# Kernel tuning notes

Hardware: AMD Instinct MI355X
Metric: run time of the kernel (lower is better)

## Reference

```python
import jax, jax.numpy as jnp
import numpy as np

B, C, Hs, Ws = 8, 512, 32, 32
NUM_HEADS, D_K = 8, 64
SCALE = D_K ** -0.5


def setup_inputs() -> dict:
    key = jax.random.key(0)
    ks = jax.random.split(key, 8)
    inner = NUM_HEADS * D_K  # 512
    s = 0.02
    return {
        "x": jax.random.normal(ks[0], (B, C, Hs, Ws), dtype=jnp.float32),
        "y": jax.random.normal(ks[1], (B, C, Hs, Ws), dtype=jnp.float32),
        "Wq": jax.random.normal(ks[2], (inner, C), dtype=jnp.float32) * s,
        "bq": jnp.zeros((inner,), dtype=jnp.float32),
        "Wkv": jax.random.normal(ks[3], (2 * inner, C), dtype=jnp.float32) * s,
        "bkv": jnp.zeros((2 * inner,), dtype=jnp.float32),
        "Wp": jax.random.normal(ks[4], (C, inner), dtype=jnp.float32) * s,
        "bp": jnp.zeros((C,), dtype=jnp.float32),
    }


def reference(x, y, Wq, bq, Wkv, bkv, Wp, bp):
    # Faithful to CrossAttentionBlock.forward: y is only shape-checked, unused.
    x_shape = x.shape
    b, c = x.shape[0], x.shape[1]
    # channel_transfer: [B, C, H, W] -> [B, H, W, C] -> [B, N, C]
    xt = jnp.transpose(x, (0, 2, 3, 1)).reshape(b, -1, c)
    n = xt.shape[1]
    # q: [B, N, H*dk] -> [B, H, N, dk]
    q = (xt @ Wq.T + bq).reshape(b, n, NUM_HEADS, D_K).transpose(0, 2, 1, 3)
    # kv: [B, N, 2*H*dk] -> [2, B, H, N, dk]
    kv = (xt @ Wkv.T + bkv).reshape(b, n, 2, NUM_HEADS, D_K).transpose(2, 0, 3, 1, 4)
    k, v = kv[0], kv[1]
    atten = jnp.einsum("bhik,bhjk->bhij", q, k) * SCALE
    atten = jax.nn.softmax(atten, axis=-1)
    res = jnp.einsum("bhij,bhjd->bhid", atten, v)  # [B, H, N, dk]
    res = res.transpose(0, 2, 1, 3).reshape(b, n, NUM_HEADS * D_K)
    res = res @ Wp.T + bp  # [B, N, C]
    # original does a raw reshape of [B, N, C] back into x_shape [B, C, H, W]
    return res.reshape(x_shape)
```

## Files before the change

kernel.cpp:

```cpp
#include <hip/hip_runtime.h>
#include <math.h>

#define BB 8
#define CC 512
#define NH 8
#define DK 64
#define NN 1024
#define MROWS (BB * NN)
#define INNER 512
#define SCALE 0.125f


typedef __attribute__((ext_vector_type(8))) short bf16x8;
typedef __attribute__((ext_vector_type(4))) float floatx4;

__device__ inline short f2bf(float f) {
    union { float f; unsigned u; } un;
    un.f = f;
    unsigned r = un.u + 0x7fffu + ((un.u >> 16) & 1u);
    return (short)(r >> 16);
}

__device__ inline short f2bf_rhu(float f) {
    union { float f; unsigned u; } un;
    un.f = f;
    return (short)((un.u + 0x8000u) >> 16);
}

#define GLD_LDS(gptr, lptr)                                                  \
    __builtin_amdgcn_global_load_lds(                                        \
        (const __attribute__((address_space(1))) void*)(gptr),               \
        (__attribute__((address_space(3))) void*)(lptr), 16, 0, 0)

__global__ __launch_bounds__(256) void prep_kernel(
    const float* __restrict__ x, const float* __restrict__ Wq,
    const float* __restrict__ Wkv, const float* __restrict__ Wp,
    const float* __restrict__ bq, const float* __restrict__ bkv,
    short* __restrict__ xtb, short* __restrict__ wqkvb,
    short* __restrict__ wpb, float* __restrict__ bqkv) {
    __shared__ float tile[32][33];
    const int bid = blockIdx.x;
    if (bid < 4096) {
        const int n0 = (bid & 31) * 32;
        const int c0 = ((bid >> 5) & 15) * 32;
        const int b = bid >> 9;
        const int tx = threadIdx.x & 31;
        const int ty = threadIdx.x >> 5;
        const float* xb = x + (size_t)b * CC * NN;
        short* xo = xtb + (size_t)b * NN * CC;
        for (int i = ty; i < 32; i += 8)
            tile[i][tx] = xb[(size_t)(c0 + i) * NN + n0 + tx];
        __syncthreads();
        for (int i = ty; i < 32; i += 8)
            xo[(size_t)(n0 + i) * CC + c0 + tx] = f2bf(tile[tx][i]);
    } else {
        const int i = (bid - 4096) * 1024 + threadIdx.x * 4;
        if (i < 786432) {
            float4 v = (i < 262144) ? *(const float4*)&Wq[i]
                                    : *(const float4*)&Wkv[i - 262144];
            wqkvb[i + 0] = f2bf(v.x);
            wqkvb[i + 1] = f2bf(v.y);
            wqkvb[i + 2] = f2bf(v.z);
            wqkvb[i + 3] = f2bf(v.w);
        } else if (i < 1048576) {
            const int j = i - 786432;
            float4 v = *(const float4*)&Wp[j];
            wpb[j + 0] = f2bf(v.x);
            wpb[j + 1] = f2bf(v.y);
            wpb[j + 2] = f2bf(v.z);
            wpb[j + 3] = f2bf(v.w);
        } else {
            const int j = i - 1048576;
            if (j < 1536) {
                float4 v = (j < 512) ? *(const float4*)&bq[j]
                                     : *(const float4*)&bkv[j - 512];
                *(float4*)&bqkv[j] = v;
            }
        }
    }
}

template <int MODE, int BN>
__global__ __launch_bounds__(256) void gemm_mfma_kernel(
    const short* __restrict__ A, const short* __restrict__ W,
    const float* __restrict__ bias, float* __restrict__ outf,
    short* __restrict__ outq, short* __restrict__ outk,
    short* __restrict__ outv) {
    constexpr int K = 512;
    constexpr int WCOLS = BN / 64;
    constexpr int WROWS = 4 / WCOLS;
    constexpr int WRSPAN = 128 / WROWS;
    constexpr int RT = WRSPAN / 16;
    constexpr int ABUF = 128 * 32;
    constexpr int BBUF = BN * 32;
    constexpr int STAGE_EL = 2 * ABUF + 2 * BBUF;
    constexpr int CS_EL = (MODE == 1) ? 128 * 132 : 0;
    constexpr int SMEM_EL = (CS_EL > STAGE_EL) ? CS_EL : STAGE_EL;
    __shared__ short smem[SMEM_EL];
    short* As = smem;
    short* Bs = smem + 2 * ABUF;

    const int t = threadIdx.x;
    const int wave = t >> 6;
    const int lane = t & 63;
    const int col = lane & 15;
    const int quad = lane >> 4;
    const int wr = wave / WCOLS;
    const int wc = wave % WCOLS;

    const int bm0 = blockIdx.x * 128;
    const int bn0 = blockIdx.y * BN;

    floatx4 acc[RT][4];
#pragma unroll
    for (int i = 0; i < RT; i++)
#pragma unroll
        for (int j = 0; j < 4; j++) acc[i][j] = (floatx4){0.f, 0.f, 0.f, 0.f};

    const int kpE = (lane & 3) * 8;
    const int rA = wave * 32 + (lane >> 2);
    const short* Ag = A + (size_t)(bm0 + rA) * K + kpE;
    const int rB = wave * (BN / 4) + (lane >> 2);
    const short* Wg = W + (size_t)(bn0 + rB) * K + kpE;
    const int aOff = wave * 1024;
    const int bOff = wave * (BN / 4) * 32;

#define GSTAGE(K0, BUF)                                                       \
    do {                                                                      \
        GLD_LDS(Ag + (K0), As + (BUF)*ABUF + aOff);                           \
        GLD_LDS(Ag + 16 * K + (K0), As + (BUF)*ABUF + aOff + 512);            \
        if constexpr (BN == 128) {                                            \
            GLD_LDS(Wg + (K0), Bs + (BUF)*BBUF + bOff);                       \
            GLD_LDS(Wg + 16 * K + (K0), Bs + (BUF)*BBUF + bOff + 512);        \
        } else {                                                              \
            GLD_LDS(Wg + (K0), Bs + (BUF)*BBUF + bOff);                       \
        }                                                                     \
    } while (0)

    GSTAGE(0, 0);

#pragma unroll
    for (int it = 0; it < 16; it++) {
        const int buf = it & 1;
        __syncthreads();
        if (it < 15) GSTAGE((it + 1) * 32, buf ^ 1);

        const short* A_ = As + buf * ABUF;
        const short* B_ = Bs + buf * BBUF;
        bf16x8 aF[RT], bF[4];
#pragma unroll
        for (int rt = 0; rt < RT; rt++)
            aF[rt] =
                *(const bf16x8*)&A_[(wr * WRSPAN + rt * 16 + col) * 32 + quad * 8];
#pragma unroll
        for (int ct = 0; ct < 4; ct++)
            bF[ct] = *(const bf16x8*)&B_[(wc * 64 + ct * 16 + col) * 32 + quad * 8];
#pragma unroll
        for (int rt = 0; rt < RT; rt++)
#pragma unroll
            for (int ct = 0; ct < 4; ct++)
                acc[rt][ct] = __builtin_amdgcn_mfma_f32_16x16x32_bf16(
                    aF[rt], bF[ct], acc[rt][ct], 0, 0, 0);
    }
#undef GSTAGE

    if (MODE == 1) {
        short* Cs = smem;
        const bool isV = (bn0 >= 1024);
        const bool isQ = (bn0 < 512);
        __syncthreads();
        if (isV) {
#pragma unroll
            for (int rt = 0; rt < RT; rt++) {
#pragma unroll
                for (int ct = 0; ct < 4; ct++) {
                    const int jn_l = wc * 64 + ct * 16 + col;
                    const float bsv = bias[bn0 + jn_l];
                    const int m_l = wr * WRSPAN + rt * 16 + quad * 4;
                    short4 v4;
                    v4.x = f2bf(acc[rt][ct][0] + bsv);
                    v4.y = f2bf(acc[rt][ct][1] + bsv);
                    v4.z = f2bf(acc[rt][ct][2] + bsv);
                    v4.w = f2bf(acc[rt][ct][3] + bsv);
                    *(short4*)&Cs[jn_l * 132 + m_l] = v4;
                }
            }
        } else {
#pragma unroll
            for (int rt = 0; rt < RT; rt++) {
#pragma unroll
                for (int ct = 0; ct < 4; ct++) {
                    const int jn_l = wc * 64 + ct * 16 + col;
                    const float bsv = bias[bn0 + jn_l];
#pragma unroll
                    for (int r = 0; r < 4; r++) {
                        const int m_l = wr * WRSPAN + rt * 16 + quad * 4 + r;
                        const float val = acc[rt][ct][r] + bsv;
                        Cs[m_l * 132 + jn_l] =
                            isQ ? f2bf(val * SCALE) : f2bf(val);
                    }
                }
            }
        }
        __syncthreads();
        const int b = bm0 >> 10;
        const int nbase = bm0 & 1023;
        if (isV) {
#pragma unroll
            for (int p = 0; p < 8; p++) {
                const int cid = p * 256 + t;
                const int jn_l = cid >> 4;
                const int m0 = (cid & 15) * 8;
                bf16x8 frag = *(const bf16x8*)&Cs[jn_l * 132 + m0];
                const int jn_g = bn0 + jn_l;
                const int h = (jn_g >> 6) & 7;
                const int d = jn_g & 63;
                *(bf16x8*)&outv[(((size_t)(b * NH + h)) * DK + d) * NN + nbase +
                                m0] = frag;
            }
        } else {
            short* dst = isQ ? outq : outk;
#pragma unroll
            for (int p = 0; p < 8; p++) {
                const int cid = p * 256 + t;
                const int m_l = cid >> 4;
                const int jn0 = (cid & 15) * 8;
                bf16x8 frag = *(const bf16x8*)&Cs[m_l * 132 + jn0];
                const int jn_g = bn0 + jn0;
                const int h = (jn_g >> 6) & 7;
                const int d = jn_g & 63;
                *(bf16x8*)&dst[(((size_t)(b * NH + h)) * NN + nbase + m_l) * DK +
                               d] = frag;
            }
        }
        return;
    }

#pragma unroll
    for (int rt = 0; rt < RT; rt++) {
#pragma unroll
        for (int ct = 0; ct < 4; ct++) {
            const int jn = bn0 + wc * 64 + ct * 16 + col;
            const float bsv = bias[jn];
#pragma unroll
            for (int r = 0; r < 4; r++) {
                const int m = bm0 + wr * WRSPAN + rt * 16 + quad * 4 + r;
                outf[(size_t)m * 512 + jn] = acc[rt][ct][r] + bsv;
            }
        }
    }
}

__global__ __launch_bounds__(256) void attn_mfma_kernel(
    const short* __restrict__ q, const short* __restrict__ k,
    const short* __restrict__ vt, short* __restrict__ out) {
    const int bh = blockIdx.x;
    const int b = bh >> 3;
    const int h = bh & 7;
    const int n0 = blockIdx.y * 128;
    const int tid = threadIdx.x;
    const int wave = tid >> 6;
    const int lane = tid & 63;
    const int col = lane & 15;
    const int quad = lane >> 4;

    __shared__ short Ks[2][64 * 64];
    __shared__ short Vs[2][64 * 64];
    __shared__ short Ps[4][32][72];

    bf16x8 qa[2][2];
#pragma unroll
    for (int rt = 0; rt < 2; rt++) {
        const size_t qoff =
            ((size_t)bh * NN + n0 + wave * 32 + rt * 16 + col) * DK;
        qa[rt][0] = *(const bf16x8*)&q[qoff + quad * 8];
        qa[rt][1] = *(const bf16x8*)&q[qoff + 32 + quad * 8];
    }

    floatx4 o[2][4];
#pragma unroll
    for (int rt = 0; rt < 2; rt++)
#pragma unroll
        for (int i = 0; i < 4; i++) o[rt][i] = (floatx4){0.f, 0.f, 0.f, 0.f};
    float l_run[2][4] = {{0.f, 0.f, 0.f, 0.f}, {0.f, 0.f, 0.f, 0.f}};

    const short* kg = k + (size_t)bh * NN * DK;
    const short* vg = vt + (size_t)bh * DK * NN;

    const int srow = lane >> 3;
    const int sunit = (lane & 7) ^ srow;
    const int sbase = wave * 16;

    const int xs = col & 7;
    const int pK0 = (quad ^ xs) * 8;
    const int pK1 = ((quad + 4) ^ xs) * 8;

#define STAGE(J0, BUF)                                                         \
    do {                                                                       \
        GLD_LDS(kg + (size_t)((J0) + sbase + srow) * DK + sunit * 8,           \
                &Ks[BUF][sbase * 64]);                                         \
        GLD_LDS(kg + (size_t)((J0) + sbase + 8 + srow) * DK + sunit * 8,       \
                &Ks[BUF][(sbase + 8) * 64]);                                   \
        GLD_LDS(vg + (size_t)(sbase + srow) * NN + (J0) + sunit * 8,           \
                &Vs[BUF][sbase * 64]);                                         \
        GLD_LDS(vg + (size_t)(sbase + 8 + srow) * NN + (J0) + sunit * 8,       \
                &Vs[BUF][(sbase + 8) * 64]);                                   \
    } while (0)

    STAGE(0, 0);

    for (int c = 0; c < 16; c++) {
        const int buf = c & 1;
        __syncthreads();
        if (c < 15) STAGE((c + 1) * 64, buf ^ 1);

        const short* K_ = &Ks[buf][0];
        const short* V_ = &Vs[buf][0];

        float p[2][4][4];
#pragma unroll
        for (int ct = 0; ct < 4; ct++) {
            bf16x8 kb0 = *(const bf16x8*)&K_[(ct * 16 + col) * 64 + pK0];
            bf16x8 kb1 = *(const bf16x8*)&K_[(ct * 16 + col) * 64 + pK1];
#pragma unroll
            for (int rt = 0; rt < 2; rt++) {
                floatx4 acc = (floatx4){0.f, 0.f, 0.f, 0.f};
                acc = __builtin_amdgcn_mfma_f32_16x16x32_bf16(qa[rt][0], kb0,
                                                              acc, 0, 0, 0);
                acc = __builtin_amdgcn_mfma_f32_16x16x32_bf16(qa[rt][1], kb1,
                                                              acc, 0, 0, 0);
#pragma unroll
                for (int r = 0; r < 4; r++) p[rt][ct][r] = __expf(acc[r]);
            }
        }

#pragma unroll
        for (int rt = 0; rt < 2; rt++)
#pragma unroll
            for (int r = 0; r < 4; r++)
                l_run[rt][r] +=
                    (p[rt][0][r] + p[rt][1][r]) + (p[rt][2][r] + p[rt][3][r]);

#pragma unroll
        for (int rt = 0; rt < 2; rt++)
#pragma unroll
            for (int ct = 0; ct < 4; ct++)
#pragma unroll
                for (int r = 0; r < 4; r++)
                    Ps[wave][rt * 16 + quad * 4 + r][ct * 16 + col] =
                        f2bf_rhu(p[rt][ct][r]);

        bf16x8 pa[2][2];
#pragma unroll
        for (int rt = 0; rt < 2; rt++) {
            pa[rt][0] = *(const bf16x8*)&Ps[wave][rt * 16 + col][quad * 8];
            pa[rt][1] = *(const bf16x8*)&Ps[wave][rt * 16 + col][32 + quad * 8];
        }

#pragma unroll
        for (int dt = 0; dt < 4; dt++) {
            bf16x8 vb0 = *(const bf16x8*)&V_[(dt * 16 + col) * 64 + pK0];
            bf16x8 vb1 = *(const bf16x8*)&V_[(dt * 16 + col) * 64 + pK1];
#pragma unroll
            for (int rt = 0; rt < 2; rt++) {
                o[rt][dt] = __builtin_amdgcn_mfma_f32_16x16x32_bf16(
                    pa[rt][0], vb0, o[rt][dt], 0, 0, 0);
                o[rt][dt] = __builtin_amdgcn_mfma_f32_16x16x32_bf16(
                    pa[rt][1], vb1, o[rt][dt], 0, 0, 0);
            }
        }
    }
#undef STAGE

    float inv[2][4];
#pragma unroll
    for (int rt = 0; rt < 2; rt++)
#pragma unroll
        for (int r = 0; r < 4; r++) {
            float lv = l_run[rt][r];
#pragma unroll
            for (int d = 1; d < 16; d <<= 1) lv += __shfl_xor(lv, d, 64);
            inv[rt][r] = 1.f / lv;
        }
#pragma unroll
    for (int rt = 0; rt < 2; rt++)
#pragma unroll
        for (int dt = 0; dt < 4; dt++)
#pragma unroll
            for (int r = 0; r < 4; r++)
                Ps[wave][rt * 16 + quad * 4 + r][dt * 16 + col] =
                    f2bf(o[rt][dt][r] * inv[rt][r]);

#pragma unroll
    for (int rt = 0; rt < 2; rt++) {
        const int row = lane >> 2;
        const int d0 = (lane & 3) * 16;
        bf16x8 f0 = *(const bf16x8*)&Ps[wave][rt * 16 + row][d0];
        bf16x8 f1 = *(const bf16x8*)&Ps[wave][rt * 16 + row][d0 + 8];
        const int m = n0 + wave * 32 + rt * 16 + row;
        short* orow = out + ((size_t)(b * NN + m)) * 512 + h * 64 + d0;
        *(bf16x8*)&orow[0] = f0;
        *(bf16x8*)&orow[8] = f1;
    }
}

extern "C" void kernel_launch(void* const* d_in, const int* in_sizes, int n_in,
                              void* d_out, int out_size, void* d_ws,
                              size_t ws_size, hipStream_t stream) {
    const float* x = (const float*)d_in[0];
    const float* Wq = (const float*)d_in[2];
    const float* bq = (const float*)d_in[3];
    const float* Wkv = (const float*)d_in[4];
    const float* bkv = (const float*)d_in[5];
    const float* Wp = (const float*)d_in[6];
    const float* bp = (const float*)d_in[7];
    float* out = (float*)d_out;

    short* ws = (short*)d_ws;
    short* xtb = ws;
    short* qb = xtb + (size_t)MROWS * CC;
    short* kb = qb + (size_t)MROWS * INNER;
    short* vb = kb + (size_t)MROWS * INNER;
    short* wqkvb = vb + (size_t)MROWS * INNER;
    short* wpb = wqkvb + (size_t)3 * INNER * CC;
    float* bqkv = (float*)(wpb + (size_t)CC * INNER);
    short* att = xtb;

    prep_kernel<<<4096 + 1026, 256, 0, stream>>>(x, Wq, Wkv, Wp, bq, bkv, xtb,
                                                 wqkvb, wpb, bqkv);
    {
        dim3 grid(MROWS / 128, (3 * INNER) / 128);
        gemm_mfma_kernel<1, 128><<<grid, 256, 0, stream>>>(
            xtb, wqkvb, bqkv, nullptr, qb, kb, vb);
    }
    {
        dim3 grid(BB * NH, NN / 128);
        attn_mfma_kernel<<<grid, 256, 0, stream>>>(qb, kb, vb, att);
    }
    {
        dim3 grid(MROWS / 128, CC / 64);
        gemm_mfma_kernel<0, 64><<<grid, 256, 0, stream>>>(
            att, wpb, bp, out, nullptr, nullptr, nullptr);
    }
}
```

Before: 152.1 us.

## Rewrite attention inner loop with 32x32x16 MFMA and register-resident P

The attention kernel switches from 16x16x32 to 32x32x16 bf16 MFMAs and computes S transposed (K times Q), so each lane holds one query column. P is packed to bf16 with v_cvt_pk_bf16_f32 and rearranged across the wave halves with v_permlane32_swap, which removes the LDS round trip through the Ps buffer and its write/read traffic. The softmax scale now folds in log2(e) so exp2 can be used in place of __expf. It relies on gfx950-specific instructions and inline asm, and the final output stores become scalar 2-byte writes instead of 16-byte vector stores.

```diff
diff --git a/kernel.cpp b/kernel.cpp
--- a/kernel.cpp
+++ b/kernel.cpp
@@ -8,11 +8,12 @@
 #define NN 1024
 #define MROWS (BB * NN)
 #define INNER 512
-#define SCALE 0.125f
+#define QSCALE 0.18033688011112042f
 
 
 typedef __attribute__((ext_vector_type(8))) short bf16x8;
 typedef __attribute__((ext_vector_type(4))) float floatx4;
+typedef __attribute__((ext_vector_type(16))) float floatx16;
 
 __device__ inline short f2bf(float f) {
     union { float f; unsigned u; } un;
@@ -21,11 +22,15 @@
     return (short)(r >> 16);
 }
 
-__device__ inline short f2bf_rhu(float f) {
-    union { float f; unsigned u; } un;
-    un.f = f;
-    return (short)((un.u + 0x8000u) >> 16);
-}
+#if defined(__has_builtin)
+#if __has_builtin(__builtin_amdgcn_exp2f)
+#define EXP2(x) __builtin_amdgcn_exp2f(x)
+#else
+#define EXP2(x) __expf((x) * 0.69314718056f)
+#endif
+#else
+#define EXP2(x) __expf((x) * 0.69314718056f)
+#endif
 
 #define GLD_LDS(gptr, lptr)                                                  \
     __builtin_amdgcn_global_load_lds(                                        \
@@ -197,7 +202,7 @@
                         const int m_l = wr * WRSPAN + rt * 16 + quad * 4 + r;
                         const float val = acc[rt][ct][r] + bsv;
                         Cs[m_l * 132 + jn_l] =
-                            isQ ? f2bf(val * SCALE) : f2bf(val);
+                            isQ ? f2bf(val * QSCALE) : f2bf(val);
                     }
                 }
             }
@@ -261,28 +266,28 @@
     const int tid = threadIdx.x;
     const int wave = tid >> 6;
     const int lane = tid & 63;
-    const int col = lane & 15;
-    const int quad = lane >> 4;
+    const int l31 = lane & 31;
+    const int hi = lane >> 5;
+    const int rsw = l31 & 7;
 
     __shared__ short Ks[2][64 * 64];
     __shared__ short Vs[2][64 * 64];
-    __shared__ short Ps[4][32][72];
-
-    bf16x8 qa[2][2];
-#pragma unroll
-    for (int rt = 0; rt < 2; rt++) {
-        const size_t qoff =
-            ((size_t)bh * NN + n0 + wave * 32 + rt * 16 + col) * DK;
-        qa[rt][0] = *(const bf16x8*)&q[qoff + quad * 8];
-        qa[rt][1] = *(const bf16x8*)&q[qoff + 32 + quad * 8];
-    }
-
-    floatx4 o[2][4];
-#pragma unroll
-    for (int rt = 0; rt < 2; rt++)
-#pragma unroll
-        for (int i = 0; i < 4; i++) o[rt][i] = (floatx4){0.f, 0.f, 0.f, 0.f};
-    float l_run[2][4] = {{0.f, 0.f, 0.f, 0.f}, {0.f, 0.f, 0.f, 0.f}};
+
+    bf16x8 qf[4];
+    {
+        const size_t qbase =
+            ((size_t)bh * NN + n0 + wave * 32 + l31) * DK + hi * 8;
+#pragma unroll
+        for (int dc = 0; dc < 4; dc++)
+            qf[dc] = *(const bf16x8*)&q[qbase + dc * 16];
+    }
+
+    floatx16 o[2];
+#pragma unroll
+    for (int dt = 0; dt < 2; dt++)
+#pragma unroll
+        for (int i = 0; i < 16; i++) o[dt][i] = 0.f;
+    float l_run = 0.f;
 
     const short* kg = k + (size_t)bh * NN * DK;
     const short* vg = vt + (size_t)bh * DK * NN;
@@ -290,10 +295,6 @@
     const int srow = lane >> 3;
     const int sunit = (lane & 7) ^ srow;
     const int sbase = wave * 16;
-
-    const int xs = col & 7;
-    const int pK0 = (quad ^ xs) * 8;
-    const int pK1 = ((quad + 4) ^ xs) * 8;
 
 #define STAGE(J0, BUF)                                                         \
     do {                                                                       \
@@ -317,91 +318,89 @@
         const short* K_ = &Ks[buf][0];
         const short* V_ = &Vs[buf][0];
 
-        float p[2][4][4];
-#pragma unroll
-        for (int ct = 0; ct < 4; ct++) {
-            bf16x8 kb0 = *(const bf16x8*)&K_[(ct * 16 + col) * 64 + pK0];
-            bf16x8 kb1 = *(const bf16x8*)&K_[(ct * 16 + col) * 64 + pK1];
-#pragma unroll
-            for (int rt = 0; rt < 2; rt++) {
-                floatx4 acc = (floatx4){0.f, 0.f, 0.f, 0.f};
-                acc = __builtin_amdgcn_mfma_f32_16x16x32_bf16(qa[rt][0], kb0,
-                                                              acc, 0, 0, 0);
-                acc = __builtin_amdgcn_mfma_f32_16x16x32_bf16(qa[rt][1], kb1,
-                                                              acc, 0, 0, 0);
-#pragma unroll
-                for (int r = 0; r < 4; r++) p[rt][ct][r] = __expf(acc[r]);
-            }
-        }
-
-#pragma unroll
-        for (int rt = 0; rt < 2; rt++)
-#pragma unroll
-            for (int r = 0; r < 4; r++)
-                l_run[rt][r] +=
-                    (p[rt][0][r] + p[rt][1][r]) + (p[rt][2][r] + p[rt][3][r]);
-
-#pragma unroll
-        for (int rt = 0; rt < 2; rt++)
-#pragma unroll
-            for (int ct = 0; ct < 4; ct++)
-#pragma unroll
-                for (int r = 0; r < 4; r++)
-                    Ps[wave][rt * 16 + quad * 4 + r][ct * 16 + col] =
-                        f2bf_rhu(p[rt][ct][r]);
-
-        bf16x8 pa[2][2];
-#pragma unroll
-        for (int rt = 0; rt < 2; rt++) {
-            pa[rt][0] = *(const bf16x8*)&Ps[wave][rt * 16 + col][quad * 8];
-            pa[rt][1] = *(const bf16x8*)&Ps[wave][rt * 16 + col][32 + quad * 8];
-        }
-
-#pragma unroll
-        for (int dt = 0; dt < 4; dt++) {
-            bf16x8 vb0 = *(const bf16x8*)&V_[(dt * 16 + col) * 64 + pK0];
-            bf16x8 vb1 = *(const bf16x8*)&V_[(dt * 16 + col) * 64 + pK1];
-#pragma unroll
-            for (int rt = 0; rt < 2; rt++) {
-                o[rt][dt] = __builtin_amdgcn_mfma_f32_16x16x32_bf16(
-                    pa[rt][0], vb0, o[rt][dt], 0, 0, 0);
-                o[rt][dt] = __builtin_amdgcn_mfma_f32_16x16x32_bf16(
-                    pa[rt][1], vb1, o[rt][dt], 0, 0, 0);
-            }
-        }
+        floatx16 sacc[2];
+#pragma unroll
+        for (int kt = 0; kt < 2; kt++) {
+#pragma unroll
+            for (int i = 0; i < 16; i++) sacc[kt][i] = 0.f;
+#pragma unroll
+            for (int dc = 0; dc < 4; dc++) {
+                bf16x8 kf = *(const bf16x8*)&K_[(kt * 32 + l31) * 64 +
+                                                (((dc * 2 + hi) ^ rsw) * 8)];
+                sacc[kt] = __builtin_amdgcn_mfma_f32_32x32x16_bf16(
+                    kf, qf[dc], sacc[kt], 0, 0, 0);
+            }
+        }
+
+        unsigned pw[2][4][2];
+#pragma unroll
+        for (int kt = 0; kt < 2; kt++) {
+            float p[16];
+#pragma unroll
+            for (int i = 0; i < 16; i++) p[i] = EXP2(sacc[kt][i]);
+            float s0 = (p[0] + p[1]) + (p[2] + p[3]);
+            float s1 = (p[4] + p[5]) + (p[6] + p[7]);
+            float s2 = (p[8] + p[9]) + (p[10] + p[11]);
+            float s3 = (p[12] + p[13]) + (p[14] + p[15]);
+            l_run += (s0 + s1) + (s2 + s3);
+#pragma unroll
+            for (int s = 0; s < 4; s++)
+#pragma unroll
+                for (int j = 0; j < 2; j++)
+                    asm("v_cvt_pk_bf16_f32 %0, %1, %2"
+                        : "=v"(pw[kt][s][j])
+                        : "v"(p[4 * s + 2 * j]), "v"(p[4 * s + 2 * j + 1]));
+#pragma unroll
+            for (int cc = 0; cc < 2; cc++)
+#pragma unroll
+                for (int j = 0; j < 2; j++)
+                    asm("v_permlane32_swap_b32 %0, %1"
+                        : "+v"(pw[kt][2 * cc][j]), "+v"(pw[kt][2 * cc + 1][j]));
+        }
+        bf16x8 PA[4];
+#pragma unroll
+        for (int kc = 0; kc < 4; kc++) {
+            const int kt = kc >> 1, cc = kc & 1;
+            union { unsigned w[4]; bf16x8 v; } pa;
+            pa.w[0] = pw[kt][2 * cc][0];
+            pa.w[1] = pw[kt][2 * cc][1];
+            pa.w[2] = pw[kt][2 * cc + 1][0];
+            pa.w[3] = pw[kt][2 * cc + 1][1];
+            PA[kc] = pa.v;
+        }
+
+#pragma unroll
+        for (int dt = 0; dt < 2; dt++)
+#pragma unroll
+            for (int kc = 0; kc < 4; kc++) {
+                bf16x8 vf = *(const bf16x8*)&V_[(dt * 32 + l31) * 64 +
+                                                (((kc * 2 + hi) ^ rsw) * 8)];
+                o[dt] = __builtin_amdgcn_mfma_f32_32x32x16_bf16(PA[kc], vf,
+                                                                o[dt], 0, 0, 0);
+            }
     }
 #undef STAGE
 
-    float inv[2][4];
-#pragma unroll
-    for (int rt = 0; rt < 2; rt++)
-#pragma unroll
-        for (int r = 0; r < 4; r++) {
-            float lv = l_run[rt][r];
-#pragma unroll
-            for (int d = 1; d < 16; d <<= 1) lv += __shfl_xor(lv, d, 64);
-            inv[rt][r] = 1.f / lv;
-        }
-#pragma unroll
-    for (int rt = 0; rt < 2; rt++)
-#pragma unroll
-        for (int dt = 0; dt < 4; dt++)
-#pragma unroll
-            for (int r = 0; r < 4; r++)
-                Ps[wave][rt * 16 + quad * 4 + r][dt * 16 + col] =
-                    f2bf(o[rt][dt][r] * inv[rt][r]);
-
-#pragma unroll
-    for (int rt = 0; rt < 2; rt++) {
-        const int row = lane >> 2;
-        const int d0 = (lane & 3) * 16;
-        bf16x8 f0 = *(const bf16x8*)&Ps[wave][rt * 16 + row][d0];
-        bf16x8 f1 = *(const bf16x8*)&Ps[wave][rt * 16 + row][d0 + 8];
-        const int m = n0 + wave * 32 + rt * 16 + row;
-        short* orow = out + ((size_t)(b * NN + m)) * 512 + h * 64 + d0;
-        *(bf16x8*)&orow[0] = f0;
-        *(bf16x8*)&orow[8] = f1;
-    }
+    l_run += __shfl_xor(l_run, 32, 64);
+    const float inv = 1.f / l_run;
+    float invq[4][4];
+#pragma unroll
+    for (int s = 0; s < 4; s++)
+#pragma unroll
+        for (int rr = 0; rr < 4; rr++)
+            invq[s][rr] = __shfl(inv, 4 * hi + rr + 8 * s, 64);
+
+#pragma unroll
+    for (int dt = 0; dt < 2; dt++)
+#pragma unroll
+        for (int s = 0; s < 4; s++)
+#pragma unroll
+            for (int rr = 0; rr < 4; rr++) {
+                const int qloc = 4 * hi + rr + 8 * s;
+                const int m = n0 + wave * 32 + qloc;
+                out[((size_t)(b * NN + m)) * 512 + h * 64 + dt * 32 + l31] =
+                    f2bf(o[dt][4 * s + rr] * invq[s][rr]);
+            }
 }
 
 extern "C" void kernel_launch(void* const* d_in, const int* in_sizes, int n_in,
```

Result: faster. 145.0 us (-4.7%).
